# Performance work log

Measured on AMD Instinct MI355X. Metric: run time of the kernel, lower is better.

## Reference

```python
import jax, jax.numpy as jnp
import numpy as np

N, D_IN, D_OUT = 65536, 1024, 256


def setup_inputs() -> dict:
    key = jax.random.key(0)
    k_x, k_wm, k_bm, k_ws, k_bs = jax.random.split(key, 5)
    x = jax.random.normal(k_x, (N, D_IN), dtype=jnp.float32)
    # nn.Linear params (stored transposed for x @ W convenience)
    W_mu = jax.random.normal(k_wm, (D_IN, D_OUT), dtype=jnp.float32) * 0.02
    b_mu = jax.random.normal(k_bm, (D_OUT,), dtype=jnp.float32) * 0.02
    W_log_std = jax.random.normal(k_ws, (D_IN, D_OUT), dtype=jnp.float32) * 0.02
    b_log_std = jax.random.normal(k_bs, (D_OUT,), dtype=jnp.float32) * 0.02
    return {"x": x, "W_mu": W_mu, "b_mu": b_mu,
            "W_log_std": W_log_std, "b_log_std": b_log_std}


def reference(x, W_mu, b_mu, W_log_std, b_log_std):
    # mean and log_std heads
    mean = x @ W_mu + b_mu                      # [n, j]
    log_std = x @ W_log_std + b_log_std         # [n, j]
    variance = jnp.exp(2.0 * log_std)           # exp(2*log_std)
    # Original builds diag covariance eye(j)*var and Cholesky-samples via
    # MultivariateNormal.rsample; for a diagonal covariance this is exactly
    # z = mean + sqrt(variance) * eps.
    eps = jax.random.normal(jax.random.key(42), mean.shape, dtype=mean.dtype)
    z = mean + jnp.sqrt(variance) * eps
    return (mean, variance, z)
```

## Files before the change

### kernel.cpp

```cpp
#include <hip/hip_runtime.h>
#include <stdint.h>

#define N_ROWS 65536
#define K_DIM  1024
#define J_OUT  256
#define ROWS_PB 32
#define NT64 16
#define THREADS 512

typedef _Float16 half8 __attribute__((ext_vector_type(8)));
typedef _Float16 half4 __attribute__((ext_vector_type(4)));
typedef float    f32x4 __attribute__((ext_vector_type(4)));

__device__ __forceinline__ uint32_t rotl32(uint32_t v, uint32_t r) {
  return __builtin_amdgcn_alignbit(v, v, 32u - r);
}
__device__ __forceinline__ uint32_t tf_bits_xor(uint32_t ctr) {
  const uint32_t ks0 = 0u, ks1 = 42u, ks2 = 0x1BD11BF0u;
  uint32_t x0 = 0u;
  uint32_t x1 = ctr + ks1;
#define TF_R(rr) x0 += x1; x1 = rotl32(x1, rr) ^ x0;
  TF_R(13) TF_R(15) TF_R(26) TF_R(6)
  x0 += ks1; x1 += ks2 + 1u;
  TF_R(17) TF_R(29) TF_R(16) TF_R(24)
  x0 += ks2; x1 += ks0 + 2u;
  TF_R(13) TF_R(15) TF_R(26) TF_R(6)
  x0 += ks0; x1 += ks1 + 3u;
  TF_R(17) TF_R(29) TF_R(16) TF_R(24)
  x0 += ks1; x1 += ks2 + 4u;
  TF_R(13) TF_R(15) TF_R(26) TF_R(6)
  x0 += ks2; x1 += ks0 + 5u;
#undef TF_R
  return x0 ^ x1;
}

__device__ __forceinline__ float eps_from_bits(uint32_t bits) {
  float f = __uint_as_float((bits >> 9) | 0x3F800000u) - 1.0f;
  float u = fmaxf(-0.99999994f, f * 2.0f - 0.99999994f);
  float w = __builtin_amdgcn_logf((1.0f - u) * (1.0f + u)) * (-0.6931471805599453f);
  float t = w - 2.5f;
  float p = 2.81022636e-08f;
  p = fmaf(p, t, 3.43273939e-07f);
  p = fmaf(p, t, -3.5233877e-06f);
  p = fmaf(p, t, -4.39150654e-06f);
  p = fmaf(p, t, 0.00021858087f);
  p = fmaf(p, t, -0.00125372503f);
  p = fmaf(p, t, -0.00417768164f);
  p = fmaf(p, t, 0.246640727f);
  p = fmaf(p, t, 1.50140941f);
  if (w >= 5.0f) {
    float s = sqrtf(w) - 3.0f;
    float q = -0.000200214257f;
    q = fmaf(q, s, 0.000100950558f);
    q = fmaf(q, s, 0.00134934322f);
    q = fmaf(q, s, -0.00367342844f);
    q = fmaf(q, s, 0.00573950773f);
    q = fmaf(q, s, -0.0076224613f);
    q = fmaf(q, s, -0.00943887047f);
    q = fmaf(q, s, 1.00167406f);
    q = fmaf(q, s, 2.83297682f);
    p = q;
  }
  return 1.41421354f * (p * u);
}

__global__ void pack_w_kernel(const float* __restrict__ Wmu,
                              const float* __restrict__ Wls,
                              _Float16* __restrict__ wt) {
  const int chunk = blockIdx.x * blockDim.x + threadIdx.x;
  const int lane = chunk & 63;
  const int n  = (chunk >> 6) & 3;
  const int ks = (chunk >> 8) & 1;
  const int w  = (chunk >> 9) & 7;
  const int t  = chunk >> 12;
  const int k0 = t * 64 + ks * 32 + (lane >> 4) * 8;
  const int c  = w * 32 + (n >> 1) * 16 + (lane & 15);
  const float* W = (n & 1) ? Wls : Wmu;
  half8 v;
#pragma unroll
  for (int e = 0; e < 8; ++e) v[e] = (_Float16)W[(size_t)(k0 + e) * J_OUT + c];
  *(half8*)(wt + (size_t)chunk * 8) = v;
}

#define KBARRIER() asm volatile("s_waitcnt lgkmcnt(0)\n\ts_barrier" ::: "memory")

#define KSTEP(T, BC, BN, SA)                                                   \
  {                                                                            \
    const _Float16* Ar_ = Abuf + ((T) & 1) * (ROWS_PB * 80);                   \
    _Float16* Aw_ = Abuf + (((T) + 1) & 1) * (ROWS_PB * 80);                   \
    if ((T) + 1 < NT64) {                                                      \
      half4 h_;                                                                \
      _Pragma("unroll") for (int e = 0; e < 4; ++e) h_[e] = (_Float16)SA[e];   \
      *(half4*)(Aw_ + swaddr) = h_;                                            \
    }                                                                          \
    if ((T) + 3 < NT64) SA = *(const f32x4*)(sp + ((T) + 3) * 64);             \
    if ((T) + 1 < NT64) {                                                      \
      const _Float16* bbn_ = bbase + (size_t)((T) + 1) * 32768;                \
      _Pragma("unroll") for (int i = 0; i < 8; ++i)                            \
        BN[i] = *(const half8*)(bbn_ + i * 512);                               \
    }                                                                          \
    half8 af0_[2], af1_[2];                                                    \
    _Pragma("unroll") for (int m = 0; m < 2; ++m) {                            \
      af0_[m] = *(const half8*)(Ar_ + arbase + m * 1280);                      \
      af1_[m] = *(const half8*)(Ar_ + arbase + m * 1280 + 32);                 \
    }                                                                          \
    _Pragma("unroll") for (int m = 0; m < 2; ++m)                              \
      _Pragma("unroll") for (int n = 0; n < 4; ++n)                            \
        acc[m][n] = __builtin_amdgcn_mfma_f32_16x16x32_f16(af0_[m], BC[n],     \
                                                           acc[m][n], 0, 0, 0);\
    _Pragma("unroll") for (int m = 0; m < 2; ++m)                              \
      _Pragma("unroll") for (int n = 0; n < 4; ++n)                            \
        acc[m][n] = __builtin_amdgcn_mfma_f32_16x16x32_f16(af1_[m], BC[4 + n], \
                                                           acc[m][n], 0, 0, 0);\
    KBARRIER();                                                                \
  }

__global__ __launch_bounds__(THREADS, 4)
void fused_heads_kernel(const float* __restrict__ x,
                        const _Float16* __restrict__ wt,
                        const float* __restrict__ b_mu,
                        const float* __restrict__ b_ls,
                        float* __restrict__ out) {
  __shared__ __align__(16) unsigned char smem[16 * 260 * 4];
  _Float16* Abuf = (_Float16*)smem;
  float*    ebuf = (float*)smem;

  const int tid  = threadIdx.x;
  const int lane = tid & 63;
  const int w    = tid >> 6;
  const int rowbase = blockIdx.x * ROWS_PB;

  const int srow = tid >> 4, skc = tid & 15;
  const float* sp = x + (size_t)(rowbase + srow) * K_DIM + skc * 4;
  const int swaddr = srow * 80 + skc * 4;

  const int arbase = (lane & 15) * 80 + (lane >> 4) * 8;
  const _Float16* bbase = wt + ((size_t)w << 12) + lane * 8;

  f32x4 acc[2][4] = {};

  {
    const f32x4 s0 = *(const f32x4*)(sp);
    half4 h;
#pragma unroll
    for (int e = 0; e < 4; ++e) h[e] = (_Float16)s0[e];
    *(half4*)(&Abuf[swaddr]) = h;
  }
  f32x4 sAa = *(const f32x4*)(sp + 64);
  f32x4 sAb = *(const f32x4*)(sp + 128);
  half8 bfA[8], bfB[8];
#pragma unroll
  for (int i = 0; i < 8; ++i) bfA[i] = *(const half8*)(bbase + i * 512);
  KBARRIER();

#pragma unroll
  for (int tt = 0; tt < 8; ++tt) {
    KSTEP(2 * tt,     bfA, bfB, sAa)
    KSTEP(2 * tt + 1, bfB, bfA, sAb)
  }

  float* out_mean = out;
  float* out_var  = out + (size_t)N_ROWS * J_OUT;
  float* out_z    = out + 2 * (size_t)N_ROWS * J_OUT;
  const int colq = lane & 15;
  const int g4   = (lane >> 4) * 4;

#pragma unroll
  for (int q = 0; q < 2; ++q) {
    const int c = w * 32 + q * 16 + colq;
    const float bm = b_mu[c];
    const float bl = b_ls[c];
#pragma unroll
    for (int m = 0; m < 2; ++m)
#pragma unroll
      for (int e = 0; e < 4; ++e) {
        acc[m][2 * q][e]     = acc[m][2 * q][e] + bm;
        acc[m][2 * q + 1][e] = __expf(2.0f * (acc[m][2 * q + 1][e] + bl));
      }
  }

#pragma unroll
  for (int m = 0; m < 2; ++m)
#pragma unroll
    for (int arr = 0; arr < 3; ++arr) {
#pragma unroll
      for (int q = 0; q < 2; ++q) {
        const int lcol = w * 32 + q * 16 + colq;
#pragma unroll
        for (int e = 0; e < 4; ++e) {
          const int lrow = g4 + e;
          float val;
          if (arr == 0) {
            val = acc[m][2 * q][e];
          } else if (arr == 1) {
            val = acc[m][2 * q + 1][e];
          } else {
            const uint32_t ctr =
                (uint32_t)((rowbase + m * 16 + lrow) * J_OUT + lcol);
            val = fmaf(sqrtf(acc[m][2 * q + 1][e]),
                       eps_from_bits(tf_bits_xor(ctr)), acc[m][2 * q][e]);
          }
          ebuf[lrow * 260 + lcol] = val;
        }
      }
      KBARRIER();
      float* oarr = (arr == 0) ? out_mean : (arr == 1) ? out_var : out_z;
#pragma unroll
      for (int i = 0; i < 2; ++i) {
        const int idx = i * THREADS + tid;
        const int r  = idx >> 6;
        const int c4 = idx & 63;
        const f32x4 v = *(const f32x4*)(ebuf + r * 260 + c4 * 4);
        *(f32x4*)(oarr + (size_t)(rowbase + m * 16 + r) * J_OUT + c4 * 4) = v;
      }
      KBARRIER();
    }
}

extern "C" void kernel_launch(void* const* d_in, const int* in_sizes, int n_in,
                              void* d_out, int out_size, void* d_ws, size_t ws_size,
                              hipStream_t stream) {
  const float* x   = (const float*)d_in[0];
  const float* Wmu = (const float*)d_in[1];
  const float* bmu = (const float*)d_in[2];
  const float* Wls = (const float*)d_in[3];
  const float* bls = (const float*)d_in[4];
  float* out = (float*)d_out;
  _Float16* wt = (_Float16*)d_ws;

  pack_w_kernel<<<256, 256, 0, stream>>>(Wmu, Wls, wt);
  fused_heads_kernel<<<N_ROWS / ROWS_PB, THREADS, 0, stream>>>(x, wt, bmu, bls, out);
}
```

Baseline: 192.9 us.

## Double rows per block to 64 so each weight fragment feeds more MFMAs

Each block now processes 64 rows instead of 32: two x row groups are staged per thread, the accumulator grows to 4x4 tiles, and each loaded weight fragment is reused across four M-tiles. This halves how often the converted fp16 weight stream is re-read per row and raises MFMA density per barrier. In exchange, register pressure roughly doubles for accumulators and prefetch buffers, and launch bounds drop to 2 blocks per SM, which lowers occupancy and reduces the number of blocks available for tail balancing.

```diff
diff --git a/kernel.cpp b/kernel.cpp
--- a/kernel.cpp
+++ b/kernel.cpp
@@ -4,7 +4,7 @@
 #define N_ROWS 65536
 #define K_DIM  1024
 #define J_OUT  256
-#define ROWS_PB 32
+#define ROWS_PB 64
 #define NT64 16
 #define THREADS 512
 
@@ -84,44 +84,47 @@
 
 #define KBARRIER() asm volatile("s_waitcnt lgkmcnt(0)\n\ts_barrier" ::: "memory")
 
-#define KSTEP(T, BC, BN, SA)                                                   \
+#define KSTEP(T, BC, BN, SA0, SA1)                                             \
   {                                                                            \
     const _Float16* Ar_ = Abuf + ((T) & 1) * (ROWS_PB * 80);                   \
     _Float16* Aw_ = Abuf + (((T) + 1) & 1) * (ROWS_PB * 80);                   \
     if ((T) + 1 < NT64) {                                                      \
-      half4 h_;                                                                \
-      _Pragma("unroll") for (int e = 0; e < 4; ++e) h_[e] = (_Float16)SA[e];   \
-      *(half4*)(Aw_ + swaddr) = h_;                                            \
-    }                                                                          \
-    if ((T) + 3 < NT64) SA = *(const f32x4*)(sp + ((T) + 3) * 64);             \
+      half4 h0_, h1_;                                                          \
+      _Pragma("unroll") for (int e = 0; e < 4; ++e) {                          \
+        h0_[e] = (_Float16)SA0[e]; h1_[e] = (_Float16)SA1[e];                  \
+      }                                                                        \
+      *(half4*)(Aw_ + swaddr) = h0_;                                           \
+      *(half4*)(Aw_ + swaddr + 32 * 80) = h1_;                                 \
+    }                                                                          \
+    if ((T) + 3 < NT64) {                                                      \
+      SA0 = *(const f32x4*)(sp0 + ((T) + 3) * 64);                             \
+      SA1 = *(const f32x4*)(sp1 + ((T) + 3) * 64);                             \
+    }                                                                          \
     if ((T) + 1 < NT64) {                                                      \
       const _Float16* bbn_ = bbase + (size_t)((T) + 1) * 32768;                \
       _Pragma("unroll") for (int i = 0; i < 8; ++i)                            \
         BN[i] = *(const half8*)(bbn_ + i * 512);                               \
     }                                                                          \
-    half8 af0_[2], af1_[2];                                                    \
-    _Pragma("unroll") for (int m = 0; m < 2; ++m) {                            \
-      af0_[m] = *(const half8*)(Ar_ + arbase + m * 1280);                      \
-      af1_[m] = *(const half8*)(Ar_ + arbase + m * 1280 + 32);                 \
-    }                                                                          \
-    _Pragma("unroll") for (int m = 0; m < 2; ++m)                              \
-      _Pragma("unroll") for (int n = 0; n < 4; ++n)                            \
-        acc[m][n] = __builtin_amdgcn_mfma_f32_16x16x32_f16(af0_[m], BC[n],     \
-                                                           acc[m][n], 0, 0, 0);\
-    _Pragma("unroll") for (int m = 0; m < 2; ++m)                              \
-      _Pragma("unroll") for (int n = 0; n < 4; ++n)                            \
-        acc[m][n] = __builtin_amdgcn_mfma_f32_16x16x32_f16(af1_[m], BC[4 + n], \
-                                                           acc[m][n], 0, 0, 0);\
+    _Pragma("unroll") for (int ks = 0; ks < 2; ++ks) {                         \
+      half8 af_[4];                                                            \
+      _Pragma("unroll") for (int m = 0; m < 4; ++m)                            \
+        af_[m] = *(const half8*)(Ar_ + arbase + m * 1280 + ks * 32);           \
+      _Pragma("unroll") for (int m = 0; m < 4; ++m)                            \
+        _Pragma("unroll") for (int n = 0; n < 4; ++n)                          \
+          acc[m][n] = __builtin_amdgcn_mfma_f32_16x16x32_f16(                  \
+              af_[m], BC[ks * 4 + n], acc[m][n], 0, 0, 0);                     \
+    }                                                                          \
     KBARRIER();                                                                \
   }
 
-__global__ __launch_bounds__(THREADS, 4)
+__global__ __launch_bounds__(THREADS, 2)
 void fused_heads_kernel(const float* __restrict__ x,
                         const _Float16* __restrict__ wt,
                         const float* __restrict__ b_mu,
                         const float* __restrict__ b_ls,
                         float* __restrict__ out) {
-  __shared__ __align__(16) unsigned char smem[16 * 260 * 4];
+  __shared__ __align__(16) unsigned char smem[ROWS_PB * 80 * 2 * 2 > 16 * 260 * 4
+                                              ? ROWS_PB * 80 * 2 * 2 : 16 * 260 * 4];
   _Float16* Abuf = (_Float16*)smem;
   float*    ebuf = (float*)smem;
 
@@ -131,23 +134,26 @@
   const int rowbase = blockIdx.x * ROWS_PB;
 
   const int srow = tid >> 4, skc = tid & 15;
-  const float* sp = x + (size_t)(rowbase + srow) * K_DIM + skc * 4;
+  const float* sp0 = x + (size_t)(rowbase + srow) * K_DIM + skc * 4;
+  const float* sp1 = sp0 + (size_t)32 * K_DIM;
   const int swaddr = srow * 80 + skc * 4;
 
   const int arbase = (lane & 15) * 80 + (lane >> 4) * 8;
   const _Float16* bbase = wt + ((size_t)w << 12) + lane * 8;
 
-  f32x4 acc[2][4] = {};
+  f32x4 acc[4][4] = {};
 
   {
-    const f32x4 s0 = *(const f32x4*)(sp);
-    half4 h;
-#pragma unroll
-    for (int e = 0; e < 4; ++e) h[e] = (_Float16)s0[e];
-    *(half4*)(&Abuf[swaddr]) = h;
-  }
-  f32x4 sAa = *(const f32x4*)(sp + 64);
-  f32x4 sAb = *(const f32x4*)(sp + 128);
+    const f32x4 s0 = *(const f32x4*)(sp0);
+    const f32x4 s1 = *(const f32x4*)(sp1);
+    half4 h0, h1;
+#pragma unroll
+    for (int e = 0; e < 4; ++e) { h0[e] = (_Float16)s0[e]; h1[e] = (_Float16)s1[e]; }
+    *(half4*)(&Abuf[swaddr]) = h0;
+    *(half4*)(&Abuf[swaddr + 32 * 80]) = h1;
+  }
+  f32x4 sAa0 = *(const f32x4*)(sp0 + 64),  sAa1 = *(const f32x4*)(sp1 + 64);
+  f32x4 sAb0 = *(const f32x4*)(sp0 + 128), sAb1 = *(const f32x4*)(sp1 + 128);
   half8 bfA[8], bfB[8];
 #pragma unroll
   for (int i = 0; i < 8; ++i) bfA[i] = *(const half8*)(bbase + i * 512);
@@ -155,8 +161,8 @@
 
 #pragma unroll
   for (int tt = 0; tt < 8; ++tt) {
-    KSTEP(2 * tt,     bfA, bfB, sAa)
-    KSTEP(2 * tt + 1, bfB, bfA, sAb)
+    KSTEP(2 * tt,     bfA, bfB, sAa0, sAa1)
+    KSTEP(2 * tt + 1, bfB, bfA, sAb0, sAb1)
   }
 
   float* out_mean = out;
@@ -171,7 +177,7 @@
     const float bm = b_mu[c];
     const float bl = b_ls[c];
 #pragma unroll
-    for (int m = 0; m < 2; ++m)
+    for (int m = 0; m < 4; ++m)
 #pragma unroll
       for (int e = 0; e < 4; ++e) {
         acc[m][2 * q][e]     = acc[m][2 * q][e] + bm;
@@ -180,7 +186,7 @@
   }
 
 #pragma unroll
-  for (int m = 0; m < 2; ++m)
+  for (int m = 0; m < 4; ++m)
 #pragma unroll
     for (int arr = 0; arr < 3; ++arr) {
 #pragma unroll
```

Measured after the change: 181.8 us. -5.7%, faster.
